# Optimization experiments

Hardware: AMD Instinct MI355X
Metric: run time of the kernel (lower is better)

## Reference

```python
import jax, jax.numpy as jnp
import numpy as np

B, N, IN_DIM, HIDDEN, N_CLASS = 32768, 25, 3, 128, 2

# BODY_25 skeleton edges from the repo
_SRC = np.array([17, 15, 18, 16, 0, 2, 3, 4, 5, 6, 7, 8, 9, 12, 10, 13, 11, 14, 23, 22, 24, 20, 19, 21])
_DST = np.array([15, 0, 16, 0, 1, 1, 2, 3, 1, 5, 6, 1, 8, 8, 9, 12, 10, 13, 22, 11, 11, 19, 14, 14])


def setup_inputs() -> dict:
    key = jax.random.key(0)
    ks = jax.random.split(key, 4)
    # skeleton edges + self loops (dgl.add_self_loop)
    src = jnp.asarray(np.concatenate([_SRC, np.arange(N)]), dtype=jnp.int64)
    dst = jnp.asarray(np.concatenate([_DST, np.arange(N)]), dtype=jnp.int64)
    return {
        "x": jax.random.normal(ks[0], (B, N, IN_DIM), dtype=jnp.float32),
        "src": src,
        "dst": dst,
        "W1": jax.random.normal(ks[1], (IN_DIM, HIDDEN), dtype=jnp.float32) / np.sqrt(IN_DIM),
        "b1": jnp.zeros((HIDDEN,), jnp.float32),
        "W2": jax.random.normal(ks[2], (HIDDEN, HIDDEN), dtype=jnp.float32) / np.sqrt(HIDDEN),
        "b2": jnp.zeros((HIDDEN,), jnp.float32),
        "Wfc": jax.random.normal(ks[3], (HIDDEN, N_CLASS), dtype=jnp.float32) / np.sqrt(HIDDEN),
        "bfc": jnp.zeros((N_CLASS,), jnp.float32),
    }


def reference(x, src, dst, W1, b1, W2, b2, Wfc, bfc):
    # x: [B, N, F] node features for B identical-topology skeleton graphs
    Bn, Nn, _ = x.shape
    ones = jnp.ones(src.shape, x.dtype)
    deg_out = jax.ops.segment_sum(ones, src, num_segments=Nn)  # [N]
    deg_in = jax.ops.segment_sum(ones, dst, num_segments=Nn)   # [N]
    # DGL GraphConv norm='both': D_in^{-1/2} A D_out^{-1/2} X W + b
    cs = jnp.where(deg_out > 0, deg_out ** -0.5, 0.0)
    ci = jnp.where(deg_in > 0, deg_in ** -0.5, 0.0)

    def gconv(h, W, b):
        msg = h[:, src, :] * cs[src][None, :, None]            # gather + src norm
        agg = jnp.zeros_like(h).at[:, dst, :].add(msg)          # scatter-add
        agg = agg * ci[None, :, None]                           # dst norm
        return agg @ W + b

    h = jax.nn.relu(gconv(x, W1, b1))
    h = jax.nn.relu(gconv(h, W2, b2))
    pooled = jnp.mean(h, axis=1)  # dgl.mean_nodes -> [B, HIDDEN]
    return pooled @ Wfc + bfc      # [B, N_CLASS]
```

## Files before the change

### kernel.cpp

```cpp
#include <hip/hip_runtime.h>

#define NN    25
#define FIN   3
#define HID   128
#define GPB   4
#define STRDQ 68

typedef int i32x4 __attribute__((ext_vector_type(4)));
typedef unsigned int uint;

__global__ void w2_absmax(const float* __restrict__ W2, uint* __restrict__ amaxbits)
{
    int i = blockIdx.x * 256 + threadIdx.x;
    float m = fabsf(W2[i]);
    #pragma unroll
    for (int off = 32; off > 0; off >>= 1)
        m = fmaxf(m, __shfl_xor(m, off));
    if ((threadIdx.x & 63) == 0)
        atomicMax(amaxbits, __float_as_uint(m));
}

static __device__ __forceinline__ long pack8(const int* q)
{
    unsigned long v = 0;
    #pragma unroll
    for (int j = 0; j < 8; ++j)
        v |= ((unsigned long)(unsigned char)(q[j] & 255)) << (8 * j);
    return (long)v;
}

__global__ void pack_w2_i8(const float* __restrict__ W2, const uint* __restrict__ amaxbits,
                           long* __restrict__ w2q)
{
    int gi = blockIdx.x * blockDim.x + threadIdx.x;
    if (gi >= 4096) return;
    int l  = gi & 63;
    int nt = (gi >> 6) & 7;
    int kt = (gi >> 9) & 3;
    int p  = gi >> 11;
    int n  = nt * 16 + (l & 15);
    int kb = kt * 32 + (l >> 4) * 8;
    float Sb = 32000.0f / __uint_as_float(*amaxbits);
    int q8[8];
    #pragma unroll
    for (int j = 0; j < 8; ++j) {
        int qv = (int)rintf(W2[(kb + j) * HID + n] * Sb);
        qv = min(max(qv, -32600), 32600);
        int lo = ((qv + 128) & 255) - 128;
        int hi = (qv - lo) >> 8;
        q8[j] = p ? lo : hi;
    }
    w2q[gi] = pack8(q8);
}

static __device__ __forceinline__ void agg25_inplace(float2* A)
{
    const float cA = 0.40824829f;
    const float cB = 0.31622777f;
    const float cC = 0.44721360f;
    const float cH = 0.5f;
    const float cS = 0.70710678f;
    A[1]  = cB * (A[0] + A[2] + A[5] + A[8]) + cC * A[1];
    A[0]  = cA * (A[15] + A[16] + A[0]);
    A[2]  = cH * (A[3]  + A[2]);
    A[3]  = cH * (A[4]  + A[3]);
    A[4]  = cS *  A[4];
    A[5]  = cH * (A[6]  + A[5]);
    A[6]  = cH * (A[7]  + A[6]);
    A[7]  = cS *  A[7];
    A[8]  = cA * (A[9] + A[12] + A[8]);
    A[9]  = cH * (A[10] + A[9]);
    A[10] = cH * (A[11] + A[10]);
    A[11] = cA * (A[22] + A[24] + A[11]);
    A[12] = cH * (A[13] + A[12]);
    A[13] = cH * (A[14] + A[13]);
    A[14] = cA * (A[19] + A[21] + A[14]);
    A[15] = cH * (A[17] + A[15]);
    A[16] = cH * (A[18] + A[16]);
    A[17] = cS *  A[17];
    A[18] = cS *  A[18];
    A[19] = cH * (A[20] + A[19]);
    A[20] = cS *  A[20];
    A[21] = cS *  A[21];
    A[22] = cH * (A[23] + A[22]);
    A[23] = cS *  A[23];
    A[24] = cS *  A[24];
}

static __device__ __forceinline__ void unpack16(uint4 d, long& hi, long& lo)
{
    uint h01 = __builtin_amdgcn_perm(d.y, d.x, 0x07050301u);
    uint h23 = __builtin_amdgcn_perm(d.w, d.z, 0x07050301u);
    uint l01 = __builtin_amdgcn_perm(d.y, d.x, 0x06040200u) ^ 0x80808080u;
    uint l23 = __builtin_amdgcn_perm(d.w, d.z, 0x06040200u) ^ 0x80808080u;
    uint hv[2] = {h01, h23};
    uint lv[2] = {l01, l23};
    __builtin_memcpy(&hi, hv, 8);
    __builtin_memcpy(&lo, lv, 8);
}

__global__ __launch_bounds__(256, 4) void gcn_main(
    const float* __restrict__ x,
    const float* __restrict__ W1, const float* __restrict__ b1,
    const float* __restrict__ b2,
    const float* __restrict__ Wfc, const float* __restrict__ bfc,
    const long* __restrict__ w2q, const uint* __restrict__ amaxbits,
    float* __restrict__ out)
{
    __shared__ __align__(16) uint  bufQ[GPB][NN][STRDQ];
    __shared__ __align__(16) float xs[GPB][80];

    const int tid  = threadIdx.x;
    const int w    = tid >> 6;
    const int lane = tid & 63;
    const int g    = blockIdx.x * GPB + w;
    const int c0   = lane * 2;

    const float* xg = x + (size_t)g * (NN * FIN);
    xs[w][lane] = xg[lane];
    if (lane < NN * FIN - 64) xs[w][64 + lane] = xg[64 + lane];
    __syncthreads();

    float2 w1r0 = *(const float2*)(W1 + 0 * HID + c0);
    float2 w1r1 = *(const float2*)(W1 + 1 * HID + c0);
    float2 w1r2 = *(const float2*)(W1 + 2 * HID + c0);
    float2 A[NN];
    const float4* xv = (const float4*)&xs[w][0];
    #pragma unroll
    for (int grp = 0; grp < 6; ++grp) {
        float4 p = xv[grp * 3 + 0];
        float4 q = xv[grp * 3 + 1];
        float4 r = xv[grp * 3 + 2];
        float xa[4][3] = {{p.x, p.y, p.z}, {p.w, q.x, q.y},
                          {q.z, q.w, r.x}, {r.y, r.z, r.w}};
        #pragma unroll
        for (int j = 0; j < 4; ++j) {
            int n = grp * 4 + j;
            A[n].x = fmaf(xa[j][0], w1r0.x, fmaf(xa[j][1], w1r1.x, xa[j][2] * w1r2.x));
            A[n].y = fmaf(xa[j][0], w1r0.y, fmaf(xa[j][1], w1r1.y, xa[j][2] * w1r2.y));
        }
    }
    {
        float x0 = xs[w][72], x1 = xs[w][73], x2 = xs[w][74];
        A[24].x = fmaf(x0, w1r0.x, fmaf(x1, w1r1.x, x2 * w1r2.x));
        A[24].y = fmaf(x0, w1r0.y, fmaf(x1, w1r1.y, x2 * w1r2.y));
    }

    float2 b1v = *(const float2*)(b1 + c0);
    agg25_inplace(A);
    #pragma unroll
    for (int n = 0; n < NN; ++n) {
        A[n].x = fmaxf(A[n].x + b1v.x, 0.0f);
        A[n].y = fmaxf(A[n].y + b1v.y, 0.0f);
    }

    agg25_inplace(A);

    float am = 1e-20f;
    #pragma unroll
    for (int n = 0; n < NN; ++n)
        am = fmaxf(am, fmaxf(fabsf(A[n].x), fabsf(A[n].y)));
    #pragma unroll
    for (int off = 32; off > 0; off >>= 1)
        am = fmaxf(am, __shfl_xor(am, off));
    const float Sa = 32000.0f / am;

    const float QLO = -32472.0f, QHI = 32728.0f;
    #pragma unroll
    for (int n = 0; n < NN; ++n) {
        float ux = fminf(QHI, fmaxf(QLO, rintf(fmaf(A[n].x, Sa, 128.0f))));
        float uy = fminf(QHI, fmaxf(QLO, rintf(fmaf(A[n].y, Sa, 128.0f))));
        uint qx = (uint)(int)ux;
        uint qy = (uint)(int)uy;
        bufQ[w][n][lane] = __builtin_amdgcn_perm(qy, qx, 0x05040100u);
    }
    __syncthreads();

    const int m0  = lane & 15;
    const int m1  = min(16 + (lane & 15), NN - 1);
    const int kq4 = (lane >> 4) * 4;

    long ah[2][4], al[2][4];
    #pragma unroll
    for (int kt = 0; kt < 4; ++kt) {
        uint4 d0 = *(const uint4*)&bufQ[w][m0][kt * 16 + kq4];
        uint4 d1 = *(const uint4*)&bufQ[w][m1][kt * 16 + kq4];
        unpack16(d0, ah[0][kt], al[0][kt]);
        unpack16(d1, ah[1][kt], al[1][kt]);
    }

    const float Sb   = 32000.0f / __uint_as_float(*amaxbits);
    const float rsL  = 256.0f / (Sa * Sb);
    const int   quad = lane >> 4;

    float s0 = 0.0f, s1 = 0.0f;
    #pragma unroll
    for (int c = 0; c < 4; ++c) {
        i32x4 aHH[2][2], aX[2][2];
        #pragma unroll
        for (int mt = 0; mt < 2; ++mt)
            #pragma unroll
            for (int i = 0; i < 2; ++i) { aHH[mt][i] = (i32x4)0; aX[mt][i] = (i32x4)0; }

        #pragma unroll
        for (int kt = 0; kt < 4; ++kt) {
            #pragma unroll
            for (int i = 0; i < 2; ++i) {
                int nt = c * 2 + i;
                long bh = w2q[(size_t)(((0 + kt) * 8 + nt) * 64 + lane)];
                long bl = w2q[(size_t)(((4 + kt) * 8 + nt) * 64 + lane)];
                aHH[0][i] = __builtin_amdgcn_mfma_i32_16x16x32_i8(ah[0][kt], bh, aHH[0][i], 0, 0, 0);
                aHH[1][i] = __builtin_amdgcn_mfma_i32_16x16x32_i8(ah[1][kt], bh, aHH[1][i], 0, 0, 0);
                aX[0][i]  = __builtin_amdgcn_mfma_i32_16x16x32_i8(ah[0][kt], bl, aX[0][i], 0, 0, 0);
                aX[0][i]  = __builtin_amdgcn_mfma_i32_16x16x32_i8(al[0][kt], bh, aX[0][i], 0, 0, 0);
                aX[1][i]  = __builtin_amdgcn_mfma_i32_16x16x32_i8(ah[1][kt], bl, aX[1][i], 0, 0, 0);
                aX[1][i]  = __builtin_amdgcn_mfma_i32_16x16x32_i8(al[1][kt], bh, aX[1][i], 0, 0, 0);
            }
        }

        #pragma unroll
        for (int i = 0; i < 2; ++i) {
            int nt  = c * 2 + i;
            int col = nt * 16 + (lane & 15);
            float b2c = b2[col];
            float s = 0.0f;
            #pragma unroll
            for (int rr = 0; rr < 4; ++rr) {
                int ci = (int)(((uint)aHH[0][i][rr] << 8)) + aX[0][i][rr];
                s += fmaxf(fmaf((float)ci, rsL, b2c), 0.0f);
            }
            #pragma unroll
            for (int rr = 0; rr < 4; ++rr) {
                int ci = (int)(((uint)aHH[1][i][rr] << 8)) + aX[1][i][rr];
                float hv = fmaxf(fmaf((float)ci, rsL, b2c), 0.0f);
                s += (quad * 4 + rr < 9) ? hv : 0.0f;
            }
            float2 wfc = *(const float2*)(Wfc + col * 2);
            s0 = fmaf(s, wfc.x, s0);
            s1 = fmaf(s, wfc.y, s1);
        }
    }

    #pragma unroll
    for (int off = 32; off > 0; off >>= 1) {
        s0 += __shfl_down(s0, off);
        s1 += __shfl_down(s1, off);
    }
    if (lane == 0) {
        out[g * 2 + 0] = s0 * (1.0f / 25.0f) + bfc[0];
        out[g * 2 + 1] = s1 * (1.0f / 25.0f) + bfc[1];
    }
}

extern "C" void kernel_launch(void* const* d_in, const int* in_sizes, int n_in,
                              void* d_out, int out_size, void* d_ws, size_t ws_size,
                              hipStream_t stream)
{
    const float* x   = (const float*)d_in[0];
    const float* W1  = (const float*)d_in[3];
    const float* b1  = (const float*)d_in[4];
    const float* W2  = (const float*)d_in[5];
    const float* b2  = (const float*)d_in[6];
    const float* Wfc = (const float*)d_in[7];
    const float* bfc = (const float*)d_in[8];
    float* out = (float*)d_out;

    const int Btot = in_sizes[0] / (NN * FIN);

    uint*  amax = (uint*)d_ws;
    long*  w2q  = (long*)((char*)d_ws + 256);

    hipMemsetAsync(amax, 0, 16, stream);
    hipLaunchKernelGGL(w2_absmax, dim3(64), dim3(256), 0, stream, W2, amax);
    hipLaunchKernelGGL(pack_w2_i8, dim3(16), dim3(256), 0, stream, W2, amax, w2q);
    hipLaunchKernelGGL(gcn_main, dim3(Btot / GPB), dim3(256), 0, stream,
                       x, W1, b1, b2, Wfc, bfc, w2q, amax, out);
}
```

Measured before the change: 182.7 us.

## Drop memset and block barriers, hoist per-column constants, single-block absmax

Replaces the memset plus atomic absmax with a single-block shared-memory reduction that also stores the precomputed W2 scale, which removes one stream operation. In the main kernel, the two __syncthreads are replaced by lgkmcnt waits because each wave only touches its own shared-memory slice. b2, Wfc, bfc and the row mask are hoisted into registers, and the activation quantization clamps are removed. Dropping the clamps could allow out-of-range values, and the hoisted constants raise register pressure.

```diff
diff --git a/kernel.cpp b/kernel.cpp
--- a/kernel.cpp
+++ b/kernel.cpp
@@ -9,15 +9,19 @@
 typedef int i32x4 __attribute__((ext_vector_type(4)));
 typedef unsigned int uint;
 
-__global__ void w2_absmax(const float* __restrict__ W2, uint* __restrict__ amaxbits)
-{
-    int i = blockIdx.x * 256 + threadIdx.x;
-    float m = fabsf(W2[i]);
-    #pragma unroll
-    for (int off = 32; off > 0; off >>= 1)
-        m = fmaxf(m, __shfl_xor(m, off));
-    if ((threadIdx.x & 63) == 0)
-        atomicMax(amaxbits, __float_as_uint(m));
+__global__ void w2_absmax(const float* __restrict__ W2, float* __restrict__ scales)
+{
+    __shared__ float red[256];
+    int tid = threadIdx.x;
+    float m = 1e-20f;
+    for (int i = tid; i < HID * HID; i += 256) m = fmaxf(m, fabsf(W2[i]));
+    red[tid] = m;
+    __syncthreads();
+    for (int s = 128; s > 0; s >>= 1) {
+        if (tid < s) red[tid] = fmaxf(red[tid], red[tid + s]);
+        __syncthreads();
+    }
+    if (tid == 0) { scales[0] = red[0]; scales[1] = 32000.0f / red[0]; }
 }
 
 static __device__ __forceinline__ long pack8(const int* q)
@@ -29,7 +33,7 @@
     return (long)v;
 }
 
-__global__ void pack_w2_i8(const float* __restrict__ W2, const uint* __restrict__ amaxbits,
+__global__ void pack_w2_i8(const float* __restrict__ W2, const float* __restrict__ scales,
                            long* __restrict__ w2q)
 {
     int gi = blockIdx.x * blockDim.x + threadIdx.x;
@@ -40,7 +44,7 @@
     int p  = gi >> 11;
     int n  = nt * 16 + (l & 15);
     int kb = kt * 32 + (l >> 4) * 8;
-    float Sb = 32000.0f / __uint_as_float(*amaxbits);
+    float Sb = scales[1];
     int q8[8];
     #pragma unroll
     for (int j = 0; j < 8; ++j) {
@@ -104,7 +108,7 @@
     const float* __restrict__ W1, const float* __restrict__ b1,
     const float* __restrict__ b2,
     const float* __restrict__ Wfc, const float* __restrict__ bfc,
-    const long* __restrict__ w2q, const uint* __restrict__ amaxbits,
+    const long* __restrict__ w2q, const float* __restrict__ scales,
     float* __restrict__ out)
 {
     __shared__ __align__(16) uint  bufQ[GPB][NN][STRDQ];
@@ -115,11 +119,27 @@
     const int lane = tid & 63;
     const int g    = blockIdx.x * GPB + w;
     const int c0   = lane * 2;
+    const int m0   = lane & 15;
+    const int quad = lane >> 4;
+
+    float  b2v[8];
+    float2 wfcv[8];
+    #pragma unroll
+    for (int nt = 0; nt < 8; ++nt) {
+        b2v[nt]  = b2[nt * 16 + m0];
+        wfcv[nt] = *(const float2*)(Wfc + (nt * 16 + m0) * 2);
+    }
+    const float  Sb   = scales[1];
+    const float2 bfcv = *(const float2*)bfc;
+    float msk1[4];
+    #pragma unroll
+    for (int rr = 0; rr < 4; ++rr)
+        msk1[rr] = (quad * 4 + rr < 9) ? 1.0f : 0.0f;
 
     const float* xg = x + (size_t)g * (NN * FIN);
     xs[w][lane] = xg[lane];
     if (lane < NN * FIN - 64) xs[w][64 + lane] = xg[64 + lane];
-    __syncthreads();
+    asm volatile("s_waitcnt lgkmcnt(0)" ::: "memory");
 
     float2 w1r0 = *(const float2*)(W1 + 0 * HID + c0);
     float2 w1r1 = *(const float2*)(W1 + 1 * HID + c0);
@@ -165,20 +185,16 @@
         am = fmaxf(am, __shfl_xor(am, off));
     const float Sa = 32000.0f / am;
 
-    const float QLO = -32472.0f, QHI = 32728.0f;
     #pragma unroll
     for (int n = 0; n < NN; ++n) {
-        float ux = fminf(QHI, fmaxf(QLO, rintf(fmaf(A[n].x, Sa, 128.0f))));
-        float uy = fminf(QHI, fmaxf(QLO, rintf(fmaf(A[n].y, Sa, 128.0f))));
-        uint qx = (uint)(int)ux;
-        uint qy = (uint)(int)uy;
+        uint qx = (uint)(int)rintf(fmaf(A[n].x, Sa, 128.0f));
+        uint qy = (uint)(int)rintf(fmaf(A[n].y, Sa, 128.0f));
         bufQ[w][n][lane] = __builtin_amdgcn_perm(qy, qx, 0x05040100u);
     }
-    __syncthreads();
-
-    const int m0  = lane & 15;
-    const int m1  = min(16 + (lane & 15), NN - 1);
-    const int kq4 = (lane >> 4) * 4;
+    asm volatile("s_waitcnt lgkmcnt(0)" ::: "memory");
+
+    const int m1  = min(16 + m0, NN - 1);
+    const int kq4 = quad * 4;
 
     long ah[2][4], al[2][4];
     #pragma unroll
@@ -189,9 +205,7 @@
         unpack16(d1, ah[1][kt], al[1][kt]);
     }
 
-    const float Sb   = 32000.0f / __uint_as_float(*amaxbits);
-    const float rsL  = 256.0f / (Sa * Sb);
-    const int   quad = lane >> 4;
+    const float rsL = 256.0f / (Sa * Sb);
 
     float s0 = 0.0f, s1 = 0.0f;
     #pragma unroll
@@ -220,9 +234,8 @@
 
         #pragma unroll
         for (int i = 0; i < 2; ++i) {
-            int nt  = c * 2 + i;
-            int col = nt * 16 + (lane & 15);
-            float b2c = b2[col];
+            int nt = c * 2 + i;
+            float b2c = b2v[nt];
             float s = 0.0f;
             #pragma unroll
             for (int rr = 0; rr < 4; ++rr) {
@@ -233,11 +246,10 @@
             for (int rr = 0; rr < 4; ++rr) {
                 int ci = (int)(((uint)aHH[1][i][rr] << 8)) + aX[1][i][rr];
                 float hv = fmaxf(fmaf((float)ci, rsL, b2c), 0.0f);
-                s += (quad * 4 + rr < 9) ? hv : 0.0f;
+                s = fmaf(hv, msk1[rr], s);
             }
-            float2 wfc = *(const float2*)(Wfc + col * 2);
-            s0 = fmaf(s, wfc.x, s0);
-            s1 = fmaf(s, wfc.y, s1);
+            s0 = fmaf(s, wfcv[nt].x, s0);
+            s1 = fmaf(s, wfcv[nt].y, s1);
         }
     }
 
@@ -247,8 +259,8 @@
         s1 += __shfl_down(s1, off);
     }
     if (lane == 0) {
-        out[g * 2 + 0] = s0 * (1.0f / 25.0f) + bfc[0];
-        out[g * 2 + 1] = s1 * (1.0f / 25.0f) + bfc[1];
+        out[g * 2 + 0] = s0 * (1.0f / 25.0f) + bfcv.x;
+        out[g * 2 + 1] = s1 * (1.0f / 25.0f) + bfcv.y;
     }
 }
 
@@ -267,12 +279,11 @@
 
     const int Btot = in_sizes[0] / (NN * FIN);
 
-    uint*  amax = (uint*)d_ws;
-    long*  w2q  = (long*)((char*)d_ws + 256);
-
-    hipMemsetAsync(amax, 0, 16, stream);
-    hipLaunchKernelGGL(w2_absmax, dim3(64), dim3(256), 0, stream, W2, amax);
-    hipLaunchKernelGGL(pack_w2_i8, dim3(16), dim3(256), 0, stream, W2, amax, w2q);
+    float* scales = (float*)d_ws;
+    long*  w2q    = (long*)((char*)d_ws + 256);
+
+    hipLaunchKernelGGL(w2_absmax, dim3(1), dim3(256), 0, stream, W2, scales);
+    hipLaunchKernelGGL(pack_w2_i8, dim3(16), dim3(256), 0, stream, W2, scales, w2q);
     hipLaunchKernelGGL(gcn_main, dim3(Btot / GPB), dim3(256), 0, stream,
-                       x, W1, b1, b2, Wfc, bfc, w2q, amax, out);
-}
+                       x, W1, b1, b2, Wfc, bfc, w2q, scales, out);
+}
```

After: 181.5 us. About the same (-0.6%).
